# Optimization experiments

Hardware: AMD Instinct MI355X
Metric: run time of the kernel (lower is better)

Reference implementation:

```python
import jax, jax.numpy as jnp
import numpy as np

N_NODES = 100000
N_EDGES = 1200000
D_IN = 64
D_HID = 64


def setup_inputs() -> dict:
    key = jax.random.key(0)
    k1, k2, k3, k4 = jax.random.split(key, 4)
    x = jax.random.normal(k1, (N_NODES, D_IN), dtype=jnp.float32)
    edge_index = jax.random.randint(k2, (2, N_EDGES), 0, N_NODES, dtype=jnp.int32)
    edge_attr = jax.random.uniform(k3, (N_EDGES,), dtype=jnp.float32)
    W = jax.random.normal(k4, (D_HID, D_IN), dtype=jnp.float32) / np.sqrt(D_IN)
    b = jnp.zeros((D_HID,), dtype=jnp.float32)
    return {"x": x, "edge_index": edge_index, "edge_attr": edge_attr, "W": W, "b": b}


def _gcn_conv(x, edge_index, edge_weight, W, b):
    # PyG GCNConv: add self-loops (weight 1), symmetric normalization,
    # linear transform, scatter-add aggregation at target (col), bias.
    n = x.shape[0]
    loop = jnp.arange(n, dtype=edge_index.dtype)
    row = jnp.concatenate([edge_index[0], loop])  # source
    col = jnp.concatenate([edge_index[1], loop])  # target
    ew = jnp.concatenate([edge_weight, jnp.ones((n,), edge_weight.dtype)])
    deg = jax.ops.segment_sum(ew, col, num_segments=n)  # [N]
    dis = jnp.where(deg > 0, jax.lax.rsqrt(deg), 0.0)
    norm = dis[row] * ew * dis[col]                     # [E+N]
    h = x @ W.T                                          # [N, D_HID]
    msg = norm[:, None] * h[row]                         # [E+N, D_HID]
    out = jax.ops.segment_sum(msg, col, num_segments=n)  # [N, D_HID]
    return out + b


def reference(x, edge_index, edge_attr, W, b):
    # layer_num=2 -> single GCNConv; dropout is identity in eval mode.
    h = _gcn_conv(x, edge_index, edge_attr, W, b)
    return jax.nn.relu(h)
```

## Files before the change

kernel.cpp:

```cpp
#include <hip/hip_runtime.h>

#define N_NODES 100000
#define N_EDGES 1200000
#define D 64
#define KP 68
#define TN 64
#define CAP 48
#define Q15 32767.0f
#define INVQ15 (1.0f / 32767.0f)
#define BW 512
#define BSH 9
#define NBKT ((N_NODES + BW - 1) / BW)
#define CAPB 8192

__device__ __forceinline__ unsigned short f2bf(float f) {
    unsigned u = __float_as_uint(f);
    return (unsigned short)((u + 0x7FFFu + ((u >> 16) & 1u)) >> 16);
}
__device__ __forceinline__ float bf2f(unsigned short h) {
    return __uint_as_float((unsigned)h << 16);
}

__global__ __launch_bounds__(256) void k_coarse(const int4* __restrict__ row4,
                                                const int4* __restrict__ col4,
                                                const float4* __restrict__ ew4,
                                                int* __restrict__ gcur,
                                                int2* __restrict__ coarse, int n4) {
    __shared__ int lcnt[NBKT];
    __shared__ int lbase[NBKT];
    int t = threadIdx.x;
    for (int i = t; i < NBKT; i += 256) lcnt[i] = 0;
    __syncthreads();

    int bkt[8]; int slot[8]; int2 rec[8];
    #pragma unroll
    for (int k = 0; k < 8; k++) bkt[k] = -1;

    #pragma unroll
    for (int r = 0; r < 2; r++) {
        int q = blockIdx.x * 512 + r * 256 + t;
        if (q < n4) {
            int4 rr = row4[q]; int4 cc = col4[q]; float4 ww = ew4[q];
            int j = r * 4;
            int c;
            c = cc.x; bkt[j+0] = c >> BSH;
            rec[j+0] = make_int2(rr.x, ((c & (BW-1)) << 15) | (int)(ww.x * Q15 + 0.5f));
            slot[j+0] = atomicAdd(&lcnt[bkt[j+0]], 1);
            c = cc.y; bkt[j+1] = c >> BSH;
            rec[j+1] = make_int2(rr.y, ((c & (BW-1)) << 15) | (int)(ww.y * Q15 + 0.5f));
            slot[j+1] = atomicAdd(&lcnt[bkt[j+1]], 1);
            c = cc.z; bkt[j+2] = c >> BSH;
            rec[j+2] = make_int2(rr.z, ((c & (BW-1)) << 15) | (int)(ww.z * Q15 + 0.5f));
            slot[j+2] = atomicAdd(&lcnt[bkt[j+2]], 1);
            c = cc.w; bkt[j+3] = c >> BSH;
            rec[j+3] = make_int2(rr.w, ((c & (BW-1)) << 15) | (int)(ww.w * Q15 + 0.5f));
            slot[j+3] = atomicAdd(&lcnt[bkt[j+3]], 1);
        }
    }
    __syncthreads();
    for (int i = t; i < NBKT; i += 256) {
        int c = lcnt[i];
        lbase[i] = c ? atomicAdd(&gcur[i], c) : 0;
    }
    __syncthreads();
    #pragma unroll
    for (int k = 0; k < 8; k++) {
        if (bkt[k] >= 0) {
            int pos = lbase[bkt[k]] + slot[k];
            if (pos < CAPB) coarse[(size_t)bkt[k] * CAPB + pos] = rec[k];
        }
    }
}

__global__ __launch_bounds__(512) void k_bin(const int* __restrict__ gcur,
                                             const int2* __restrict__ coarse,
                                             int* __restrict__ cnt,
                                             float* __restrict__ dis,
                                             unsigned int* __restrict__ em, int n_nodes) {
    __shared__ int   cur512[BW];
    __shared__ float d512[BW];
    int b = blockIdx.x, t = threadIdx.x;
    int total = min(gcur[b], CAPB);
    int nbase = b * BW;
    int bw = min(BW, n_nodes - nbase);
    for (int i = t; i < BW; i += 512) { cur512[i] = 0; d512[i] = 0.f; }
    __syncthreads();
    const int2* src = &coarse[(size_t)b * CAPB];
    for (int i = t; i < total; i += 512) {
        int2 r = src[i];
        int cl = (r.y >> 15) & (BW - 1);
        float w = (float)(r.y & 0x7FFF) * INVQ15;
        int s = atomicAdd(&cur512[cl], 1);
        atomicAdd(&d512[cl], w);
        if (s < CAP)
            em[(size_t)(nbase + cl) * CAP + s] = ((unsigned)r.x << 15) | (unsigned)(r.y & 0x7FFF);
    }
    __syncthreads();
    for (int i = t; i < bw; i += 512) {
        cnt[nbase + i] = cur512[i];
        dis[nbase + i] = rsqrtf(1.0f + d512[i]);
    }
}

#define AGG_STEP(rec, accv)                                                          \
    {                                                                                \
        float hh = bf2f(hsb[(size_t)((rec) >> 15) * D + l]);                         \
        accv = fmaf((float)((rec) & 0x7FFFu) * INVQ15, hh, accv);                    \
    }
__global__ __launch_bounds__(256) void k_agg_cap(const int* __restrict__ cnt,
                                                 const unsigned int* __restrict__ em,
                                                 const unsigned short* __restrict__ hsb,
                                                 const float* __restrict__ dis,
                                                 const float* __restrict__ b,
                                                 float* __restrict__ out, int n_nodes) {
    int w = threadIdx.x >> 6, l = threadIdx.x & 63;
    int n0 = blockIdx.x * 8 + w * 2;
    int n1 = n0 + 1;
    int c0 = min(cnt[n0], CAP);
    int c1 = min(cnt[n1], CAP);
    int recs0 = (int)em[(size_t)n0 * CAP + min(l, max(c0 - 1, 0))];
    int recs1 = (int)em[(size_t)n1 * CAP + min(l, max(c1 - 1, 0))];
    float acc0 = bf2f(hsb[(size_t)n0 * D + l]);
    float acc1 = bf2f(hsb[(size_t)n1 * D + l]);

    int i0 = 0, i1 = 0;
    while (i0 + 4 <= c0 && i1 + 4 <= c1) {
        unsigned a0 = (unsigned)__shfl(recs0, i0 + 0);
        unsigned a1 = (unsigned)__shfl(recs0, i0 + 1);
        unsigned a2 = (unsigned)__shfl(recs0, i0 + 2);
        unsigned a3 = (unsigned)__shfl(recs0, i0 + 3);
        unsigned b0 = (unsigned)__shfl(recs1, i1 + 0);
        unsigned b1 = (unsigned)__shfl(recs1, i1 + 1);
        unsigned b2 = (unsigned)__shfl(recs1, i1 + 2);
        unsigned b3 = (unsigned)__shfl(recs1, i1 + 3);
        float ha0 = bf2f(hsb[(size_t)(a0 >> 15) * D + l]);
        float ha1 = bf2f(hsb[(size_t)(a1 >> 15) * D + l]);
        float ha2 = bf2f(hsb[(size_t)(a2 >> 15) * D + l]);
        float ha3 = bf2f(hsb[(size_t)(a3 >> 15) * D + l]);
        float hb0 = bf2f(hsb[(size_t)(b0 >> 15) * D + l]);
        float hb1 = bf2f(hsb[(size_t)(b1 >> 15) * D + l]);
        float hb2 = bf2f(hsb[(size_t)(b2 >> 15) * D + l]);
        float hb3 = bf2f(hsb[(size_t)(b3 >> 15) * D + l]);
        acc0 = fmaf((float)(a0 & 0x7FFFu) * INVQ15, ha0, acc0);
        acc0 = fmaf((float)(a1 & 0x7FFFu) * INVQ15, ha1, acc0);
        acc0 = fmaf((float)(a2 & 0x7FFFu) * INVQ15, ha2, acc0);
        acc0 = fmaf((float)(a3 & 0x7FFFu) * INVQ15, ha3, acc0);
        acc1 = fmaf((float)(b0 & 0x7FFFu) * INVQ15, hb0, acc1);
        acc1 = fmaf((float)(b1 & 0x7FFFu) * INVQ15, hb1, acc1);
        acc1 = fmaf((float)(b2 & 0x7FFFu) * INVQ15, hb2, acc1);
        acc1 = fmaf((float)(b3 & 0x7FFFu) * INVQ15, hb3, acc1);
        i0 += 4; i1 += 4;
    }
    for (; i0 + 4 <= c0; i0 += 4) {
        unsigned a0 = (unsigned)__shfl(recs0, i0 + 0);
        unsigned a1 = (unsigned)__shfl(recs0, i0 + 1);
        unsigned a2 = (unsigned)__shfl(recs0, i0 + 2);
        unsigned a3 = (unsigned)__shfl(recs0, i0 + 3);
        float ha0 = bf2f(hsb[(size_t)(a0 >> 15) * D + l]);
        float ha1 = bf2f(hsb[(size_t)(a1 >> 15) * D + l]);
        float ha2 = bf2f(hsb[(size_t)(a2 >> 15) * D + l]);
        float ha3 = bf2f(hsb[(size_t)(a3 >> 15) * D + l]);
        acc0 = fmaf((float)(a0 & 0x7FFFu) * INVQ15, ha0, acc0);
        acc0 = fmaf((float)(a1 & 0x7FFFu) * INVQ15, ha1, acc0);
        acc0 = fmaf((float)(a2 & 0x7FFFu) * INVQ15, ha2, acc0);
        acc0 = fmaf((float)(a3 & 0x7FFFu) * INVQ15, ha3, acc0);
    }
    for (; i0 < c0; i0++) {
        unsigned a = (unsigned)__shfl(recs0, i0);
        AGG_STEP(a, acc0);
    }
    for (; i1 + 4 <= c1; i1 += 4) {
        unsigned b0 = (unsigned)__shfl(recs1, i1 + 0);
        unsigned b1 = (unsigned)__shfl(recs1, i1 + 1);
        unsigned b2 = (unsigned)__shfl(recs1, i1 + 2);
        unsigned b3 = (unsigned)__shfl(recs1, i1 + 3);
        float hb0 = bf2f(hsb[(size_t)(b0 >> 15) * D + l]);
        float hb1 = bf2f(hsb[(size_t)(b1 >> 15) * D + l]);
        float hb2 = bf2f(hsb[(size_t)(b2 >> 15) * D + l]);
        float hb3 = bf2f(hsb[(size_t)(b3 >> 15) * D + l]);
        acc1 = fmaf((float)(b0 & 0x7FFFu) * INVQ15, hb0, acc1);
        acc1 = fmaf((float)(b1 & 0x7FFFu) * INVQ15, hb1, acc1);
        acc1 = fmaf((float)(b2 & 0x7FFFu) * INVQ15, hb2, acc1);
        acc1 = fmaf((float)(b3 & 0x7FFFu) * INVQ15, hb3, acc1);
    }
    for (; i1 < c1; i1++) {
        unsigned bb = (unsigned)__shfl(recs1, i1);
        AGG_STEP(bb, acc1);
    }

    float bl = b[l];
    float v0 = fmaf(dis[n0], acc0, bl);
    float v1 = fmaf(dis[n1], acc1, bl);
    out[(size_t)n0 * D + l] = v0 > 0.f ? v0 : 0.f;
    out[(size_t)n1 * D + l] = v1 > 0.f ? v1 : 0.f;
}

__global__ __launch_bounds__(256) void k_gemm_tile(const float* __restrict__ x,
                                                   const float* __restrict__ W,
                                                   const float* __restrict__ dis,
                                                   unsigned short* __restrict__ hsb, int n_nodes) {
    __shared__ float wt[D * KP];
    int t = threadIdx.x;
    int base = blockIdx.x * TN;
    #pragma unroll
    for (int c = 0; c < 16; c++) {
        int idx = t + c * 256;
        wt[(idx & 63) * KP + (idx >> 6)] = W[idx];
    }
    __syncthreads();

    int tx = t & 15, ty = t >> 4;
    int f0 = tx * 4, n0 = base + ty * 4;
    const float* xr0 = x + (size_t)min(n0 + 0, n_nodes - 1) * D;
    const float* xr1 = x + (size_t)min(n0 + 1, n_nodes - 1) * D;
    const float* xr2 = x + (size_t)min(n0 + 2, n_nodes - 1) * D;
    const float* xr3 = x + (size_t)min(n0 + 3, n_nodes - 1) * D;

    float acc[4][4] = {};
    #pragma unroll 4
    for (int k = 0; k < D; k += 4) {
        float a[4][4], wv[4][4];
        *(float4*)a[0] = *(const float4*)&xr0[k];
        *(float4*)a[1] = *(const float4*)&xr1[k];
        *(float4*)a[2] = *(const float4*)&xr2[k];
        *(float4*)a[3] = *(const float4*)&xr3[k];
        #pragma unroll
        for (int kk = 0; kk < 4; kk++)
            *(float4*)wv[kk] = *(const float4*)&wt[(k + kk) * KP + f0];
        #pragma unroll
        for (int kk = 0; kk < 4; kk++)
            #pragma unroll
            for (int j = 0; j < 4; j++)
                #pragma unroll
                for (int ff = 0; ff < 4; ff++)
                    acc[j][ff] = fmaf(a[j][kk], wv[kk][ff], acc[j][ff]);
    }
    #pragma unroll
    for (int j = 0; j < 4; j++) {
        int n = n0 + j;
        if (n < n_nodes) {
            float dv = dis[n];
            unsigned short h0 = f2bf(dv * acc[j][0]);
            unsigned short h1 = f2bf(dv * acc[j][1]);
            unsigned short h2 = f2bf(dv * acc[j][2]);
            unsigned short h3 = f2bf(dv * acc[j][3]);
            uint2 pk;
            pk.x = (unsigned)h0 | ((unsigned)h1 << 16);
            pk.y = (unsigned)h2 | ((unsigned)h3 << 16);
            *(uint2*)&hsb[(size_t)n * D + f0] = pk;
        }
    }
}

extern "C" void kernel_launch(void* const* d_in, const int* in_sizes, int n_in,
                              void* d_out, int out_size, void* d_ws, size_t ws_size,
                              hipStream_t stream) {
    const float* x   = (const float*)d_in[0];
    const int*   ei  = (const int*)d_in[1];
    const float* ew  = (const float*)d_in[2];
    const float* W   = (const float*)d_in[3];
    const float* b   = (const float*)d_in[4];
    float* out = (float*)d_out;

    const int* row = ei;
    const int* col = ei + N_EDGES;

    char* p = (char*)d_ws;
    auto carve = [&](size_t bytes) { char* q = p; p += (bytes + 255) & ~(size_t)255; return q; };
    float*          dis    = (float*)carve(N_NODES * sizeof(float));
    unsigned short* hsb    = (unsigned short*)carve((size_t)N_NODES * D * sizeof(unsigned short));
    int*            cnt    = (int*)  carve(N_NODES * sizeof(int));
    unsigned int*   em     = (unsigned int*)carve((size_t)N_NODES * CAP * sizeof(unsigned int));
    int*            gcur   = (int*)  carve(NBKT * sizeof(int));
    int2*           coarse = (int2*) carve((size_t)NBKT * CAPB * sizeof(int2));

    hipMemsetAsync(gcur, 0, NBKT * sizeof(int), stream);

    int n4 = N_EDGES / 4;
    int nbA = (n4 + 511) / 512;
    k_coarse<<<nbA, 256, 0, stream>>>(
        (const int4*)row, (const int4*)col, (const float4*)ew, gcur, coarse, n4);
    k_bin<<<NBKT, 512, 0, stream>>>(gcur, coarse, cnt, dis, em, N_NODES);
    k_gemm_tile<<<(N_NODES + TN - 1) / TN, 256, 0, stream>>>(x, W, dis, hsb, N_NODES);
    k_agg_cap<<<N_NODES / 8, 256, 0, stream>>>(cnt, em, hsb, dis, b, out, N_NODES);
}
```

Measured before the change: 169.8 us.

## Fuse GEMM into edge-binning kernel and move source normalization into aggregation

The GEMM is merged into the coarse-binning kernel as extra blocks, so the feature transform no longer waits on degree computation and one launch is removed. To make that possible, the source-side rsqrt(deg) scaling is taken out of the stored bf16 features and applied per edge in the aggregation through a gather from dis. This removes a kernel launch and lets the GEMM overlap with binning. In exchange, aggregation does an extra random 4-byte load per edge, and the fused kernel's larger shared-memory footprint may lower occupancy for the binning blocks.

```diff
diff --git a/kernel.cpp b/kernel.cpp
--- a/kernel.cpp
+++ b/kernel.cpp
@@ -12,6 +12,9 @@
 #define BSH 9
 #define NBKT ((N_NODES + BW - 1) / BW)
 #define CAPB 8192
+#define N4 (N_EDGES / 4)
+#define NB_COARSE ((N4 + 511) / 512)
+#define NB_GEMM ((N_NODES + TN - 1) / TN)
 
 __device__ __forceinline__ unsigned short f2bf(float f) {
     unsigned u = __float_as_uint(f);
@@ -21,53 +24,110 @@
     return __uint_as_float((unsigned)h << 16);
 }
 
-__global__ __launch_bounds__(256) void k_coarse(const int4* __restrict__ row4,
-                                                const int4* __restrict__ col4,
-                                                const float4* __restrict__ ew4,
-                                                int* __restrict__ gcur,
-                                                int2* __restrict__ coarse, int n4) {
+__global__ __launch_bounds__(256) void k_pre(const int4* __restrict__ row4,
+                                             const int4* __restrict__ col4,
+                                             const float4* __restrict__ ew4,
+                                             int* __restrict__ gcur,
+                                             int2* __restrict__ coarse,
+                                             const float* __restrict__ x,
+                                             const float* __restrict__ W,
+                                             unsigned short* __restrict__ hb,
+                                             int n4, int n_nodes) {
     __shared__ int lcnt[NBKT];
     __shared__ int lbase[NBKT];
+    __shared__ float wt[D * KP];
     int t = threadIdx.x;
-    for (int i = t; i < NBKT; i += 256) lcnt[i] = 0;
-    __syncthreads();
-
-    int bkt[8]; int slot[8]; int2 rec[8];
-    #pragma unroll
-    for (int k = 0; k < 8; k++) bkt[k] = -1;
-
-    #pragma unroll
-    for (int r = 0; r < 2; r++) {
-        int q = blockIdx.x * 512 + r * 256 + t;
-        if (q < n4) {
-            int4 rr = row4[q]; int4 cc = col4[q]; float4 ww = ew4[q];
-            int j = r * 4;
-            int c;
-            c = cc.x; bkt[j+0] = c >> BSH;
-            rec[j+0] = make_int2(rr.x, ((c & (BW-1)) << 15) | (int)(ww.x * Q15 + 0.5f));
-            slot[j+0] = atomicAdd(&lcnt[bkt[j+0]], 1);
-            c = cc.y; bkt[j+1] = c >> BSH;
-            rec[j+1] = make_int2(rr.y, ((c & (BW-1)) << 15) | (int)(ww.y * Q15 + 0.5f));
-            slot[j+1] = atomicAdd(&lcnt[bkt[j+1]], 1);
-            c = cc.z; bkt[j+2] = c >> BSH;
-            rec[j+2] = make_int2(rr.z, ((c & (BW-1)) << 15) | (int)(ww.z * Q15 + 0.5f));
-            slot[j+2] = atomicAdd(&lcnt[bkt[j+2]], 1);
-            c = cc.w; bkt[j+3] = c >> BSH;
-            rec[j+3] = make_int2(rr.w, ((c & (BW-1)) << 15) | (int)(ww.w * Q15 + 0.5f));
-            slot[j+3] = atomicAdd(&lcnt[bkt[j+3]], 1);
-        }
-    }
-    __syncthreads();
-    for (int i = t; i < NBKT; i += 256) {
-        int c = lcnt[i];
-        lbase[i] = c ? atomicAdd(&gcur[i], c) : 0;
-    }
-    __syncthreads();
-    #pragma unroll
-    for (int k = 0; k < 8; k++) {
-        if (bkt[k] >= 0) {
-            int pos = lbase[bkt[k]] + slot[k];
-            if (pos < CAPB) coarse[(size_t)bkt[k] * CAPB + pos] = rec[k];
+
+    if (blockIdx.x < NB_COARSE) {
+        for (int i = t; i < NBKT; i += 256) lcnt[i] = 0;
+        __syncthreads();
+
+        int bkt[8]; int slot[8]; int2 rec[8];
+        #pragma unroll
+        for (int k = 0; k < 8; k++) bkt[k] = -1;
+
+        #pragma unroll
+        for (int r = 0; r < 2; r++) {
+            int q = blockIdx.x * 512 + r * 256 + t;
+            if (q < n4) {
+                int4 rr = row4[q]; int4 cc = col4[q]; float4 ww = ew4[q];
+                int j = r * 4;
+                int c;
+                c = cc.x; bkt[j+0] = c >> BSH;
+                rec[j+0] = make_int2(rr.x, ((c & (BW-1)) << 15) | (int)(ww.x * Q15 + 0.5f));
+                slot[j+0] = atomicAdd(&lcnt[bkt[j+0]], 1);
+                c = cc.y; bkt[j+1] = c >> BSH;
+                rec[j+1] = make_int2(rr.y, ((c & (BW-1)) << 15) | (int)(ww.y * Q15 + 0.5f));
+                slot[j+1] = atomicAdd(&lcnt[bkt[j+1]], 1);
+                c = cc.z; bkt[j+2] = c >> BSH;
+                rec[j+2] = make_int2(rr.z, ((c & (BW-1)) << 15) | (int)(ww.z * Q15 + 0.5f));
+                slot[j+2] = atomicAdd(&lcnt[bkt[j+2]], 1);
+                c = cc.w; bkt[j+3] = c >> BSH;
+                rec[j+3] = make_int2(rr.w, ((c & (BW-1)) << 15) | (int)(ww.w * Q15 + 0.5f));
+                slot[j+3] = atomicAdd(&lcnt[bkt[j+3]], 1);
+            }
+        }
+        __syncthreads();
+        for (int i = t; i < NBKT; i += 256) {
+            int c = lcnt[i];
+            lbase[i] = c ? atomicAdd(&gcur[i], c) : 0;
+        }
+        __syncthreads();
+        #pragma unroll
+        for (int k = 0; k < 8; k++) {
+            if (bkt[k] >= 0) {
+                int pos = lbase[bkt[k]] + slot[k];
+                if (pos < CAPB) coarse[(size_t)bkt[k] * CAPB + pos] = rec[k];
+            }
+        }
+    } else {
+        int base = (blockIdx.x - NB_COARSE) * TN;
+        #pragma unroll
+        for (int c = 0; c < 16; c++) {
+            int idx = t + c * 256;
+            wt[(idx & 63) * KP + (idx >> 6)] = W[idx];
+        }
+        __syncthreads();
+
+        int tx = t & 15, ty = t >> 4;
+        int f0 = tx * 4, n0 = base + ty * 4;
+        const float* xr0 = x + (size_t)min(n0 + 0, n_nodes - 1) * D;
+        const float* xr1 = x + (size_t)min(n0 + 1, n_nodes - 1) * D;
+        const float* xr2 = x + (size_t)min(n0 + 2, n_nodes - 1) * D;
+        const float* xr3 = x + (size_t)min(n0 + 3, n_nodes - 1) * D;
+
+        float acc[4][4] = {};
+        #pragma unroll 4
+        for (int k = 0; k < D; k += 4) {
+            float a[4][4], wv[4][4];
+            *(float4*)a[0] = *(const float4*)&xr0[k];
+            *(float4*)a[1] = *(const float4*)&xr1[k];
+            *(float4*)a[2] = *(const float4*)&xr2[k];
+            *(float4*)a[3] = *(const float4*)&xr3[k];
+            #pragma unroll
+            for (int kk = 0; kk < 4; kk++)
+                *(float4*)wv[kk] = *(const float4*)&wt[(k + kk) * KP + f0];
+            #pragma unroll
+            for (int kk = 0; kk < 4; kk++)
+                #pragma unroll
+                for (int j = 0; j < 4; j++)
+                    #pragma unroll
+                    for (int ff = 0; ff < 4; ff++)
+                        acc[j][ff] = fmaf(a[j][kk], wv[kk][ff], acc[j][ff]);
+        }
+        #pragma unroll
+        for (int j = 0; j < 4; j++) {
+            int n = n0 + j;
+            if (n < n_nodes) {
+                unsigned short h0 = f2bf(acc[j][0]);
+                unsigned short h1 = f2bf(acc[j][1]);
+                unsigned short h2 = f2bf(acc[j][2]);
+                unsigned short h3 = f2bf(acc[j][3]);
+                uint2 pk;
+                pk.x = (unsigned)h0 | ((unsigned)h1 << 16);
+                pk.y = (unsigned)h2 | ((unsigned)h3 << 16);
+                *(uint2*)&hb[(size_t)n * D + f0] = pk;
+            }
         }
     }
 }
@@ -102,14 +162,9 @@
     }
 }
 
-#define AGG_STEP(rec, accv)                                                          \
-    {                                                                                \
-        float hh = bf2f(hsb[(size_t)((rec) >> 15) * D + l]);                         \
-        accv = fmaf((float)((rec) & 0x7FFFu) * INVQ15, hh, accv);                    \
-    }
 __global__ __launch_bounds__(256) void k_agg_cap(const int* __restrict__ cnt,
                                                  const unsigned int* __restrict__ em,
-                                                 const unsigned short* __restrict__ hsb,
+                                                 const unsigned short* __restrict__ hb,
                                                  const float* __restrict__ dis,
                                                  const float* __restrict__ b,
                                                  float* __restrict__ out, int n_nodes) {
@@ -120,8 +175,9 @@
     int c1 = min(cnt[n1], CAP);
     int recs0 = (int)em[(size_t)n0 * CAP + min(l, max(c0 - 1, 0))];
     int recs1 = (int)em[(size_t)n1 * CAP + min(l, max(c1 - 1, 0))];
-    float acc0 = bf2f(hsb[(size_t)n0 * D + l]);
-    float acc1 = bf2f(hsb[(size_t)n1 * D + l]);
+    float ds0 = dis[n0], ds1 = dis[n1];
+    float acc0 = ds0 * bf2f(hb[(size_t)n0 * D + l]);
+    float acc1 = ds1 * bf2f(hb[(size_t)n1 * D + l]);
 
     int i0 = 0, i1 = 0;
     while (i0 + 4 <= c0 && i1 + 4 <= c1) {
@@ -133,22 +189,30 @@
         unsigned b1 = (unsigned)__shfl(recs1, i1 + 1);
         unsigned b2 = (unsigned)__shfl(recs1, i1 + 2);
         unsigned b3 = (unsigned)__shfl(recs1, i1 + 3);
-        float ha0 = bf2f(hsb[(size_t)(a0 >> 15) * D + l]);
-        float ha1 = bf2f(hsb[(size_t)(a1 >> 15) * D + l]);
-        float ha2 = bf2f(hsb[(size_t)(a2 >> 15) * D + l]);
-        float ha3 = bf2f(hsb[(size_t)(a3 >> 15) * D + l]);
-        float hb0 = bf2f(hsb[(size_t)(b0 >> 15) * D + l]);
-        float hb1 = bf2f(hsb[(size_t)(b1 >> 15) * D + l]);
-        float hb2 = bf2f(hsb[(size_t)(b2 >> 15) * D + l]);
-        float hb3 = bf2f(hsb[(size_t)(b3 >> 15) * D + l]);
-        acc0 = fmaf((float)(a0 & 0x7FFFu) * INVQ15, ha0, acc0);
-        acc0 = fmaf((float)(a1 & 0x7FFFu) * INVQ15, ha1, acc0);
-        acc0 = fmaf((float)(a2 & 0x7FFFu) * INVQ15, ha2, acc0);
-        acc0 = fmaf((float)(a3 & 0x7FFFu) * INVQ15, ha3, acc0);
-        acc1 = fmaf((float)(b0 & 0x7FFFu) * INVQ15, hb0, acc1);
-        acc1 = fmaf((float)(b1 & 0x7FFFu) * INVQ15, hb1, acc1);
-        acc1 = fmaf((float)(b2 & 0x7FFFu) * INVQ15, hb2, acc1);
-        acc1 = fmaf((float)(b3 & 0x7FFFu) * INVQ15, hb3, acc1);
+        float ha0 = bf2f(hb[(size_t)(a0 >> 15) * D + l]);
+        float ha1 = bf2f(hb[(size_t)(a1 >> 15) * D + l]);
+        float ha2 = bf2f(hb[(size_t)(a2 >> 15) * D + l]);
+        float ha3 = bf2f(hb[(size_t)(a3 >> 15) * D + l]);
+        float hb0 = bf2f(hb[(size_t)(b0 >> 15) * D + l]);
+        float hb1 = bf2f(hb[(size_t)(b1 >> 15) * D + l]);
+        float hb2 = bf2f(hb[(size_t)(b2 >> 15) * D + l]);
+        float hb3 = bf2f(hb[(size_t)(b3 >> 15) * D + l]);
+        float wa0 = (float)(a0 & 0x7FFFu) * INVQ15 * dis[a0 >> 15];
+        float wa1 = (float)(a1 & 0x7FFFu) * INVQ15 * dis[a1 >> 15];
+        float wa2 = (float)(a2 & 0x7FFFu) * INVQ15 * dis[a2 >> 15];
+        float wa3 = (float)(a3 & 0x7FFFu) * INVQ15 * dis[a3 >> 15];
+        float wb0 = (float)(b0 & 0x7FFFu) * INVQ15 * dis[b0 >> 15];
+        float wb1 = (float)(b1 & 0x7FFFu) * INVQ15 * dis[b1 >> 15];
+        float wb2 = (float)(b2 & 0x7FFFu) * INVQ15 * dis[b2 >> 15];
+        float wb3 = (float)(b3 & 0x7FFFu) * INVQ15 * dis[b3 >> 15];
+        acc0 = fmaf(wa0, ha0, acc0);
+        acc0 = fmaf(wa1, ha1, acc0);
+        acc0 = fmaf(wa2, ha2, acc0);
+        acc0 = fmaf(wa3, ha3, acc0);
+        acc1 = fmaf(wb0, hb0, acc1);
+        acc1 = fmaf(wb1, hb1, acc1);
+        acc1 = fmaf(wb2, hb2, acc1);
+        acc1 = fmaf(wb3, hb3, acc1);
         i0 += 4; i1 += 4;
     }
     for (; i0 + 4 <= c0; i0 += 4) {
@@ -156,100 +220,45 @@
         unsigned a1 = (unsigned)__shfl(recs0, i0 + 1);
         unsigned a2 = (unsigned)__shfl(recs0, i0 + 2);
         unsigned a3 = (unsigned)__shfl(recs0, i0 + 3);
-        float ha0 = bf2f(hsb[(size_t)(a0 >> 15) * D + l]);
-        float ha1 = bf2f(hsb[(size_t)(a1 >> 15) * D + l]);
-        float ha2 = bf2f(hsb[(size_t)(a2 >> 15) * D + l]);
-        float ha3 = bf2f(hsb[(size_t)(a3 >> 15) * D + l]);
-        acc0 = fmaf((float)(a0 & 0x7FFFu) * INVQ15, ha0, acc0);
-        acc0 = fmaf((float)(a1 & 0x7FFFu) * INVQ15, ha1, acc0);
-        acc0 = fmaf((float)(a2 & 0x7FFFu) * INVQ15, ha2, acc0);
-        acc0 = fmaf((float)(a3 & 0x7FFFu) * INVQ15, ha3, acc0);
+        float ha0 = bf2f(hb[(size_t)(a0 >> 15) * D + l]);
+        float ha1 = bf2f(hb[(size_t)(a1 >> 15) * D + l]);
+        float ha2 = bf2f(hb[(size_t)(a2 >> 15) * D + l]);
+        float ha3 = bf2f(hb[(size_t)(a3 >> 15) * D + l]);
+        acc0 = fmaf((float)(a0 & 0x7FFFu) * INVQ15 * dis[a0 >> 15], ha0, acc0);
+        acc0 = fmaf((float)(a1 & 0x7FFFu) * INVQ15 * dis[a1 >> 15], ha1, acc0);
+        acc0 = fmaf((float)(a2 & 0x7FFFu) * INVQ15 * dis[a2 >> 15], ha2, acc0);
+        acc0 = fmaf((float)(a3 & 0x7FFFu) * INVQ15 * dis[a3 >> 15], ha3, acc0);
     }
     for (; i0 < c0; i0++) {
         unsigned a = (unsigned)__shfl(recs0, i0);
-        AGG_STEP(a, acc0);
+        acc0 = fmaf((float)(a & 0x7FFFu) * INVQ15 * dis[a >> 15],
+                    bf2f(hb[(size_t)(a >> 15) * D + l]), acc0);
     }
     for (; i1 + 4 <= c1; i1 += 4) {
         unsigned b0 = (unsigned)__shfl(recs1, i1 + 0);
         unsigned b1 = (unsigned)__shfl(recs1, i1 + 1);
         unsigned b2 = (unsigned)__shfl(recs1, i1 + 2);
         unsigned b3 = (unsigned)__shfl(recs1, i1 + 3);
-        float hb0 = bf2f(hsb[(size_t)(b0 >> 15) * D + l]);
-        float hb1 = bf2f(hsb[(size_t)(b1 >> 15) * D + l]);
-        float hb2 = bf2f(hsb[(size_t)(b2 >> 15) * D + l]);
-        float hb3 = bf2f(hsb[(size_t)(b3 >> 15) * D + l]);
-        acc1 = fmaf((float)(b0 & 0x7FFFu) * INVQ15, hb0, acc1);
-        acc1 = fmaf((float)(b1 & 0x7FFFu) * INVQ15, hb1, acc1);
-        acc1 = fmaf((float)(b2 & 0x7FFFu) * INVQ15, hb2, acc1);
-        acc1 = fmaf((float)(b3 & 0x7FFFu) * INVQ15, hb3, acc1);
+        float hb0 = bf2f(hb[(size_t)(b0 >> 15) * D + l]);
+        float hb1 = bf2f(hb[(size_t)(b1 >> 15) * D + l]);
+        float hb2 = bf2f(hb[(size_t)(b2 >> 15) * D + l]);
+        float hb3 = bf2f(hb[(size_t)(b3 >> 15) * D + l]);
+        acc1 = fmaf((float)(b0 & 0x7FFFu) * INVQ15 * dis[b0 >> 15], hb0, acc1);
+        acc1 = fmaf((float)(b1 & 0x7FFFu) * INVQ15 * dis[b1 >> 15], hb1, acc1);
+        acc1 = fmaf((float)(b2 & 0x7FFFu) * INVQ15 * dis[b2 >> 15], hb2, acc1);
+        acc1 = fmaf((float)(b3 & 0x7FFFu) * INVQ15 * dis[b3 >> 15], hb3, acc1);
     }
     for (; i1 < c1; i1++) {
         unsigned bb = (unsigned)__shfl(recs1, i1);
-        AGG_STEP(bb, acc1);
+        acc1 = fmaf((float)(bb & 0x7FFFu) * INVQ15 * dis[bb >> 15],
+                    bf2f(hb[(size_t)(bb >> 15) * D + l]), acc1);
     }
 
     float bl = b[l];
-    float v0 = fmaf(dis[n0], acc0, bl);
-    float v1 = fmaf(dis[n1], acc1, bl);
+    float v0 = fmaf(ds0, acc0, bl);
+    float v1 = fmaf(ds1, acc1, bl);
     out[(size_t)n0 * D + l] = v0 > 0.f ? v0 : 0.f;
     out[(size_t)n1 * D + l] = v1 > 0.f ? v1 : 0.f;
-}
-
-__global__ __launch_bounds__(256) void k_gemm_tile(const float* __restrict__ x,
-                                                   const float* __restrict__ W,
-                                                   const float* __restrict__ dis,
-                                                   unsigned short* __restrict__ hsb, int n_nodes) {
-    __shared__ float wt[D * KP];
-    int t = threadIdx.x;
-    int base = blockIdx.x * TN;
-    #pragma unroll
-    for (int c = 0; c < 16; c++) {
-        int idx = t + c * 256;
-        wt[(idx & 63) * KP + (idx >> 6)] = W[idx];
-    }
-    __syncthreads();
-
-    int tx = t & 15, ty = t >> 4;
-    int f0 = tx * 4, n0 = base + ty * 4;
-    const float* xr0 = x + (size_t)min(n0 + 0, n_nodes - 1) * D;
-    const float* xr1 = x + (size_t)min(n0 + 1, n_nodes - 1) * D;
-    const float* xr2 = x + (size_t)min(n0 + 2, n_nodes - 1) * D;
-    const float* xr3 = x + (size_t)min(n0 + 3, n_nodes - 1) * D;
-
-    float acc[4][4] = {};
-    #pragma unroll 4
-    for (int k = 0; k < D; k += 4) {
-        float a[4][4], wv[4][4];
-        *(float4*)a[0] = *(const float4*)&xr0[k];
-        *(float4*)a[1] = *(const float4*)&xr1[k];
-        *(float4*)a[2] = *(const float4*)&xr2[k];
-        *(float4*)a[3] = *(const float4*)&xr3[k];
-        #pragma unroll
-        for (int kk = 0; kk < 4; kk++)
-            *(float4*)wv[kk] = *(const float4*)&wt[(k + kk) * KP + f0];
-        #pragma unroll
-        for (int kk = 0; kk < 4; kk++)
-            #pragma unroll
-            for (int j = 0; j < 4; j++)
-                #pragma unroll
-                for (int ff = 0; ff < 4; ff++)
-                    acc[j][ff] = fmaf(a[j][kk], wv[kk][ff], acc[j][ff]);
-    }
-    #pragma unroll
-    for (int j = 0; j < 4; j++) {
-        int n = n0 + j;
-        if (n < n_nodes) {
-            float dv = dis[n];
-            unsigned short h0 = f2bf(dv * acc[j][0]);
-            unsigned short h1 = f2bf(dv * acc[j][1]);
-            unsigned short h2 = f2bf(dv * acc[j][2]);
-            unsigned short h3 = f2bf(dv * acc[j][3]);
-            uint2 pk;
-            pk.x = (unsigned)h0 | ((unsigned)h1 << 16);
-            pk.y = (unsigned)h2 | ((unsigned)h3 << 16);
-            *(uint2*)&hsb[(size_t)n * D + f0] = pk;
-        }
-    }
 }
 
 extern "C" void kernel_launch(void* const* d_in, const int* in_sizes, int n_in,
@@ -268,7 +277,7 @@
     char* p = (char*)d_ws;
     auto carve = [&](size_t bytes) { char* q = p; p += (bytes + 255) & ~(size_t)255; return q; };
     float*          dis    = (float*)carve(N_NODES * sizeof(float));
-    unsigned short* hsb    = (unsigned short*)carve((size_t)N_NODES * D * sizeof(unsigned short));
+    unsigned short* hb     = (unsigned short*)carve((size_t)N_NODES * D * sizeof(unsigned short));
     int*            cnt    = (int*)  carve(N_NODES * sizeof(int));
     unsigned int*   em     = (unsigned int*)carve((size_t)N_NODES * CAP * sizeof(unsigned int));
     int*            gcur   = (int*)  carve(NBKT * sizeof(int));
@@ -276,11 +285,9 @@
 
     hipMemsetAsync(gcur, 0, NBKT * sizeof(int), stream);
 
-    int n4 = N_EDGES / 4;
-    int nbA = (n4 + 511) / 512;
-    k_coarse<<<nbA, 256, 0, stream>>>(
-        (const int4*)row, (const int4*)col, (const float4*)ew, gcur, coarse, n4);
+    k_pre<<<NB_COARSE + NB_GEMM, 256, 0, stream>>>(
+        (const int4*)row, (const int4*)col, (const float4*)ew, gcur, coarse,
+        x, W, hb, N4, N_NODES);
     k_bin<<<NBKT, 512, 0, stream>>>(gcur, coarse, cnt, dis, em, N_NODES);
-    k_gemm_tile<<<(N_NODES + TN - 1) / TN, 256, 0, stream>>>(x, W, dis, hsb, N_NODES);
-    k_agg_cap<<<N_NODES / 8, 256, 0, stream>>>(cnt, em, hsb, dis, b, out, N_NODES);
-}
+    k_agg_cap<<<N_NODES / 8, 256, 0, stream>>>(cnt, em, hb, dis, b, out, N_NODES);
+}
```

After: 167.5 us. No clear change (-1.4%).
